# Performance work log

Hardware: AMD Instinct MI355X
Metric: run time of the kernel (lower is better)

## Reference

```python
import jax, jax.numpy as jnp
import numpy as np

B, NX, NC, C, H = 4, 1024, 2048, 1024, 16
DH = C // H            # head_dim = 64
SCALE = DH ** -0.5


def setup_inputs() -> dict:
    key = jax.random.key(0)
    ks = jax.random.split(key, 6)
    # sorted unique token indices to update per batch (== positions where update_mask==1)
    rng = np.random.default_rng(0)
    idx = np.stack([np.sort(rng.permutation(NC)[:NX]) for _ in range(B)]).astype(np.int32)
    return {
        "x": jax.random.normal(ks[0], (B, NX, C), jnp.float32),
        "update_idx": jnp.asarray(idx),                              # (B, NX) int32
        "cache_k": jax.random.normal(ks[1], (B, H, NC, DH), jnp.float32),
        "cache_v": jax.random.normal(ks[2], (B, H, NC, DH), jnp.float32),
        "w_qkv": jax.random.normal(ks[3], (3 * C, C), jnp.float32) * 0.02,
        "b_qkv": jnp.zeros((3 * C,), jnp.float32),
        "w_proj": jax.random.normal(ks[4], (C, C), jnp.float32) * 0.02,
        "b_proj": jnp.zeros((C,), jnp.float32),
    }


def reference(x, update_idx, cache_k, cache_v, w_qkv, b_qkv, w_proj, b_proj):
    Bq, N, Cq = x.shape
    # QKV projection: (B, N, 3C) -> (3, B, H, N, Dh) layout as in torch permute(2,0,3,1,4)
    qkv = (x @ w_qkv.T + b_qkv).reshape(Bq, N, 3, H, DH)
    q = qkv[:, :, 0].transpose(0, 2, 1, 3)  # (B, H, N, Dh)
    k = qkv[:, :, 1].transpose(0, 2, 1, 3)
    v = qkv[:, :, 2].transpose(0, 2, 1, 3)
    # masked_scatter_ of k/v into cache at the masked (updated) token slots.
    # Indices are sorted, so row-order masked_scatter == indexed scatter.
    scat = jax.vmap(lambda cache, idx, src: cache.at[:, idx, :].set(src))
    k_full = scat(cache_k, update_idx, k)    # (B, H, NC, Dh)
    v_full = scat(cache_v, update_idx, v)
    # plain attention: q scaled, full softmax over cache length
    attn = jax.nn.softmax(jnp.einsum('bhqd,bhkd->bhqk', q * SCALE, k_full), axis=-1)
    out = jnp.einsum('bhqk,bhkd->bhqd', attn, v_full)  # (B, H, N, Dh)
    out = out.transpose(0, 2, 1, 3).reshape(Bq, N, Cq)
    return out @ w_proj.T + b_proj
```

## Files before the change

kernel.cpp:

```cpp
#include <hip/hip_runtime.h>
#include <hip/hip_bf16.h>

#define B_   4
#define NX_  1024
#define NC_  2048
#define C_   1024
#define H_   16
#define DH_  64

typedef __attribute__((ext_vector_type(8))) __bf16 bf16x8;
typedef __attribute__((ext_vector_type(4))) float  f32x4;

static __device__ __forceinline__ unsigned short f2bf(float f) {
    unsigned int u = __float_as_uint(f);
    u += 0x7fffu + ((u >> 16) & 1u);
    return (unsigned short)(u >> 16);
}

static __device__ __forceinline__ unsigned int pk2(float lo, float hi) {
    unsigned int a = __float_as_uint(lo) + 0x8000u;
    unsigned int b = __float_as_uint(hi) + 0x8000u;
    return __builtin_amdgcn_perm(b, a, 0x07060302);
}

static __device__ __forceinline__ bf16x8 ldfrag(const unsigned short* p) {
    union { uint4 u; bf16x8 b; } cv;
    cv.u = *reinterpret_cast<const uint4*>(p);
    return cv.b;
}

__global__ __launch_bounds__(256) void cvt_all_kernel(
    const float* __restrict__ x,  const float* __restrict__ wq,
    const float* __restrict__ wp, const float* __restrict__ ck,
    const float* __restrict__ cv_,
    unsigned short* __restrict__ xbf,  unsigned short* __restrict__ wqbf,
    unsigned short* __restrict__ wpbf, unsigned short* __restrict__ kfb,
    unsigned short* __restrict__ vt) {
    int blk = blockIdx.x;
    if (blk < 16384) {
        const float* src; unsigned short* dst; int i;
        if (blk < 4096)      { src = x;  dst = xbf;  i = blk; }
        else if (blk < 7168) { src = wq; dst = wqbf; i = blk - 4096; }
        else if (blk < 8192) { src = wp; dst = wpbf; i = blk - 7168; }
        else                 { src = ck; dst = kfb;  i = blk - 8192; }
        int idx = i * 256 + threadIdx.x;
        float4 f = reinterpret_cast<const float4*>(src)[idx];
        ushort4 o;
        o.x = f2bf(f.x); o.y = f2bf(f.y); o.z = f2bf(f.z); o.w = f2bf(f.w);
        reinterpret_cast<ushort4*>(dst)[idx] = o;
    } else {
        int i   = blk - 16384;
        int t   = threadIdx.x;
        int bh  = i >> 6;
        int kg  = i & 63;
        int d   = t & 63;
        int kci = t >> 6;
        int kc  = kg * 4 + kci;
        const float* src = cv_ + ((size_t)bh * NC_ + (size_t)kc * 8) * DH_ + d;
        union { uint4 u; unsigned short s[8]; } o;
#pragma unroll
        for (int j = 0; j < 8; j++) o.s[j] = f2bf(src[(size_t)j * DH_]);
        *reinterpret_cast<uint4*>(vt + ((size_t)bh * DH_ + d) * NC_ + (size_t)kc * 8) = o.u;
    }
}

#define LSTR 40

__global__ __launch_bounds__(256, 3) void qkv_gemm_kernel(
    const unsigned short* __restrict__ xbf,
    const unsigned short* __restrict__ wbf,
    const float* __restrict__ bias,
    const int* __restrict__ uidx,
    unsigned short* __restrict__ qb,
    unsigned short* __restrict__ kf,
    unsigned short* __restrict__ vt)
{
    __shared__ unsigned short As[128 * LSTR], Bs[128 * LSTR];
    __shared__ int jtab[128];
    int bn = blockIdx.x, bm = blockIdx.y;
    int w = threadIdx.x >> 6, l = threadIdx.x & 63;
    int quad = l >> 4, col = l & 15;
    int wr = w >> 1, wc = w & 1;
    int srow = w * 32 + (l >> 2), schk = (l & 3) * 8;

    const unsigned short* Ap = xbf + (size_t)(bm * 128 + srow) * C_ + schk;
    const unsigned short* Bp = wbf + (size_t)(bn * 128 + srow) * C_ + schk;
    unsigned short* Aw = As + srow * LSTR + schk;
    unsigned short* Bw = Bs + srow * LSTR + schk;

    f32x4 acc[4][4];
#pragma unroll
    for (int a = 0; a < 4; a++)
#pragma unroll
        for (int b = 0; b < 4; b++) acc[a][b] = (f32x4){0.f, 0.f, 0.f, 0.f};

    uint4 ar0, ar1, br0, br1;
#define LDREG(kk_)                                                       \
    {   int kk = (kk_) * 32;                                             \
        ar0 = *reinterpret_cast<const uint4*>(Ap + kk);                  \
        ar1 = *reinterpret_cast<const uint4*>(Ap + 16 * C_ + kk);        \
        br0 = *reinterpret_cast<const uint4*>(Bp + kk);                  \
        br1 = *reinterpret_cast<const uint4*>(Bp + 16 * C_ + kk);        \
    }
#define WRTILE()                                                         \
    {   *reinterpret_cast<uint4*>(Aw)             = ar0;                 \
        *reinterpret_cast<uint4*>(Aw + 16 * LSTR) = ar1;                 \
        *reinterpret_cast<uint4*>(Bw)             = br0;                 \
        *reinterpret_cast<uint4*>(Bw + 16 * LSTR) = br1;                 \
    }

    LDREG(0);
    WRTILE();
    LDREG(1);
    __syncthreads();
#pragma unroll 1
    for (int it = 0; it < 32; it++) {
        bf16x8 af[4], bfr[4];
#pragma unroll
        for (int t = 0; t < 4; t++) af[t]  = ldfrag(&As[(wr * 64 + t * 16 + col) * LSTR + quad * 8]);
#pragma unroll
        for (int t = 0; t < 4; t++) bfr[t] = ldfrag(&Bs[(wc * 64 + t * 16 + col) * LSTR + quad * 8]);
#pragma unroll
        for (int mt = 0; mt < 4; mt++)
#pragma unroll
            for (int nt = 0; nt < 4; nt++)
                acc[mt][nt] = __builtin_amdgcn_mfma_f32_16x16x32_bf16(af[mt], bfr[nt], acc[mt][nt], 0, 0, 0);
        if (it < 31) {
            __syncthreads();
            WRTILE();
            LDREG(it + 2 < 31 ? it + 2 : 31);
            __syncthreads();
        }
    }
#undef LDREG
#undef WRTILE

    int part = bn >> 3;
    float bv[4];
#pragma unroll
    for (int nt = 0; nt < 4; nt++) bv[nt] = bias[bn * 128 + wc * 64 + nt * 16 + col];

    if (part <= 1) {
        int nl[4];
#pragma unroll
        for (int nt = 0; nt < 4; nt++) nl[nt] = (bn * 128 + wc * 64 + nt * 16 + col) & 1023;
        const float QS = 0.18033688011112042f;
#pragma unroll
        for (int mt = 0; mt < 4; mt++)
#pragma unroll
            for (int r = 0; r < 4; r++) {
                int m = bm * 128 + wr * 64 + mt * 16 + quad * 4 + r;
                int b = m >> 10, i = m & 1023;
                int j = (part == 0) ? 0 : uidx[m];
#pragma unroll
                for (int nt = 0; nt < 4; nt++) {
                    int h = nl[nt] >> 6, d = nl[nt] & 63;
                    float v = acc[mt][nt][r] + bv[nt];
                    if (part == 0)
                        qb[((size_t)(b * H_ + h) * NX_ + i) * DH_ + d] = f2bf(v * QS);
                    else
                        kf[((size_t)(b * H_ + h) * NC_ + j) * DH_ + d] = f2bf(v);
                }
            }
    } else {
        if (threadIdx.x < 128) jtab[threadIdx.x] = uidx[bm * 128 + threadIdx.x];
        __syncthreads();
        int h = ((bn * 128 + wc * 64) & 1023) >> 6;
        int b = (bm * 128) >> 10;
        unsigned short* T = (wc == 0) ? As : Bs;
        int jv = jtab[wr * 64 + l];
        unsigned short* vb2 = vt + ((size_t)(b * H_ + h) * 64) * NC_ + jv;
#pragma unroll 1
        for (int round = 0; round < 2; round++) {
            if (wr == round) {
#pragma unroll
                for (int nt = 0; nt < 4; nt++)
#pragma unroll
                    for (int mt = 0; mt < 4; mt++) {
                        uint2 pk;
                        pk.x = pk2(acc[mt][nt][0] + bv[nt], acc[mt][nt][1] + bv[nt]);
                        pk.y = pk2(acc[mt][nt][2] + bv[nt], acc[mt][nt][3] + bv[nt]);
                        *reinterpret_cast<uint2*>(&T[(nt * 16 + col) * 72 + mt * 16 + quad * 4]) = pk;
                    }
                asm volatile("s_waitcnt lgkmcnt(0)" ::: "memory");
#pragma unroll 1
                for (int d = 0; d < 64; d++)
                    vb2[(size_t)d * NC_] = T[d * 72 + l];
            }
            __syncthreads();
        }
    }
}

#define PST 40
__global__ __launch_bounds__(256, 4) void attn_kernel(
    const unsigned short* __restrict__ qb,
    const unsigned short* __restrict__ kf,
    const unsigned short* __restrict__ vt,
    unsigned short* __restrict__ ao)
{
    __shared__ __align__(16) char smem[20480 + 10240];
    unsigned short* Klo = (unsigned short*)smem;
    unsigned short* Khi = Klo + 64 * LSTR;
    unsigned short* V0s = Khi + 64 * LSTR;
    unsigned short* V1s = V0s + 64 * LSTR;
    unsigned short* Psh = (unsigned short*)(smem + 20480);
    float* Om = (float*)smem;
    float* Lm = Om + 2 * 32 * 64;

    int id = blockIdx.x;
    int qt = (id >> 3) & 15;
    int bh = ((id >> 7) << 3) | (id & 7);
    int wave = threadIdx.x >> 6, lane = threadIdx.x & 63;
    int quad = lane >> 4, col = lane & 15;
    int qh = wave & 1;
    int kh = wave >> 1;
    int srow = wave * 16 + (lane >> 2), schk = (lane & 3) * 8;

    const unsigned short* qrow0 = qb + ((size_t)bh * NX_ + qt * 64 + qh * 32 + col) * DH_;
    bf16x8 qfA[2], qfB[2];
    qfA[0] = ldfrag(qrow0 + quad * 8);
    qfB[0] = ldfrag(qrow0 + 32 + quad * 8);
    qfA[1] = ldfrag(qrow0 + 16 * DH_ + quad * 8);
    qfB[1] = ldfrag(qrow0 + 16 * DH_ + 32 + quad * 8);

    const unsigned short* Kp = kf + ((size_t)bh * NC_ + srow) * DH_ + schk;
    const unsigned short* Vp = vt + ((size_t)bh * DH_ + srow) * NC_ + schk;
    unsigned short* Kwl = Klo + srow * LSTR + schk;
    unsigned short* Kwh = Khi + srow * LSTR + schk;
    unsigned short* Vw0 = V0s + srow * LSTR + schk;
    unsigned short* Vw1 = V1s + srow * LSTR + schk;
    unsigned short* Pw0 = Psh + (wave * 2 + 0) * 16 * PST;
    unsigned short* Pw1 = Psh + (wave * 2 + 1) * 16 * PST;
    const unsigned short* Vs = kh ? V1s : V0s;
    int kq = kh * 32;

    f32x4 o[4][2];
#pragma unroll
    for (int m = 0; m < 4; m++)
#pragma unroll
        for (int n = 0; n < 2; n++) o[m][n] = (f32x4){0.f, 0.f, 0.f, 0.f};
    float l_i[2] = {0.f, 0.f};

    uint4 kr0, kr1, vr0, vr1;
#define LDREG(kb_)                                                        \
    {   kr0 = *reinterpret_cast<const uint4*>(Kp + (size_t)(kb_) * 64 * DH_);      \
        kr1 = *reinterpret_cast<const uint4*>(Kp + (size_t)(kb_) * 64 * DH_ + 32); \
        vr0 = *reinterpret_cast<const uint4*>(Vp + (kb_) * 64);           \
        vr1 = *reinterpret_cast<const uint4*>(Vp + (kb_) * 64 + 32);      \
    }
#define WRTILE()                                                          \
    {   *reinterpret_cast<uint4*>(Kwl) = kr0;                             \
        *reinterpret_cast<uint4*>(Kwh) = kr1;                             \
        *reinterpret_cast<uint4*>(Vw0) = vr0;                             \
        *reinterpret_cast<uint4*>(Vw1) = vr1;                             \
    }

    LDREG(0);
    WRTILE();
    LDREG(1);
    __syncthreads();

#pragma unroll 1
    for (int kb = 0; kb < 32; kb++) {
        f32x4 s[2][2];
#pragma unroll
        for (int mt = 0; mt < 2; mt++)
#pragma unroll
            for (int nt = 0; nt < 2; nt++) s[mt][nt] = (f32x4){0.f, 0.f, 0.f, 0.f};
#pragma unroll
        for (int mt = 0; mt < 2; mt++) {
            bf16x8 ka = ldfrag(&Klo[(kq + mt * 16 + col) * LSTR + quad * 8]);
            bf16x8 kb_ = ldfrag(&Khi[(kq + mt * 16 + col) * LSTR + quad * 8]);
#pragma unroll
            for (int nt = 0; nt < 2; nt++) {
                s[mt][nt] = __builtin_amdgcn_mfma_f32_16x16x32_bf16(ka,  qfA[nt], s[mt][nt], 0, 0, 0);
                s[mt][nt] = __builtin_amdgcn_mfma_f32_16x16x32_bf16(kb_, qfB[nt], s[mt][nt], 0, 0, 0);
            }
        }
        bf16x8 vfr[4];
#pragma unroll
        for (int t = 0; t < 4; t++) vfr[t] = ldfrag(&Vs[(t * 16 + col) * LSTR + quad * 8]);
#pragma unroll
        for (int nt = 0; nt < 2; nt++) {
            unsigned short* Pw = nt ? Pw1 : Pw0;
            float p0 = exp2f(s[0][nt][0]), p1 = exp2f(s[0][nt][1]);
            float p2 = exp2f(s[0][nt][2]), p3 = exp2f(s[0][nt][3]);
            float p4 = exp2f(s[1][nt][0]), p5 = exp2f(s[1][nt][1]);
            float p6 = exp2f(s[1][nt][2]), p7 = exp2f(s[1][nt][3]);
            l_i[nt] += ((p0 + p1) + (p2 + p3)) + ((p4 + p5) + (p6 + p7));
            uint2 w0; w0.x = pk2(p0, p1); w0.y = pk2(p2, p3);
            uint2 w1; w1.x = pk2(p4, p5); w1.y = pk2(p6, p7);
            *reinterpret_cast<uint2*>(&Pw[col * PST +      quad * 4]) = w0;
            *reinterpret_cast<uint2*>(&Pw[col * PST + 16 + quad * 4]) = w1;
        }
        asm volatile("" ::: "memory");
        {
            bf16x8 pf0 = ldfrag(&Pw0[col * PST + quad * 8]);
            bf16x8 pf1 = ldfrag(&Pw1[col * PST + quad * 8]);
#pragma unroll
            for (int mt = 0; mt < 4; mt++) {
                o[mt][0] = __builtin_amdgcn_mfma_f32_16x16x32_bf16(vfr[mt], pf0, o[mt][0], 0, 0, 0);
                o[mt][1] = __builtin_amdgcn_mfma_f32_16x16x32_bf16(vfr[mt], pf1, o[mt][1], 0, 0, 0);
            }
        }
        asm volatile("" ::: "memory");
        if (kb < 31) {
            __syncthreads();
            WRTILE();
            LDREG(kb + 2 < 31 ? kb + 2 : 31);
            __syncthreads();
        }
    }
#undef LDREG
#undef WRTILE

#pragma unroll
    for (int nt = 0; nt < 2; nt++) {
        l_i[nt] += __shfl_xor(l_i[nt], 16, 64);
        l_i[nt] += __shfl_xor(l_i[nt], 32, 64);
    }

    __syncthreads();
    if (kh == 1) {
#pragma unroll
        for (int mt = 0; mt < 4; mt++)
#pragma unroll
            for (int nt = 0; nt < 2; nt++)
#pragma unroll
                for (int r = 0; r < 4; r++)
                    Om[(qh * 32 + (mt * 2 + nt) * 4 + r) * 64 + lane] = o[mt][nt][r];
        if (quad == 0) {
            Lm[(qh * 2 + 0) * 16 + col] = l_i[0];
            Lm[(qh * 2 + 1) * 16 + col] = l_i[1];
        }
    }
    __syncthreads();
    if (kh == 0) {
        float inv[2];
#pragma unroll
        for (int nt = 0; nt < 2; nt++)
            inv[nt] = 1.f / (l_i[nt] + Lm[(qh * 2 + nt) * 16 + col]);
        int b = bh >> 4, h = bh & 15;
#pragma unroll
        for (int mt = 0; mt < 4; mt++)
#pragma unroll
            for (int nt = 0; nt < 2; nt++) {
                int base = (qh * 32 + (mt * 2 + nt) * 4) * 64 + lane;
                float v0 = (o[mt][nt][0] + Om[base])       * inv[nt];
                float v1 = (o[mt][nt][1] + Om[base + 64])  * inv[nt];
                float v2 = (o[mt][nt][2] + Om[base + 128]) * inv[nt];
                float v3 = (o[mt][nt][3] + Om[base + 192]) * inv[nt];
                int q = qt * 64 + qh * 32 + nt * 16 + col;
                uint2 ov;
                ov.x = pk2(v0, v1);
                ov.y = pk2(v2, v3);
                *reinterpret_cast<uint2*>(ao + ((size_t)b * NX_ + q) * C_ +
                                          h * 64 + mt * 16 + quad * 4) = ov;
            }
    }
}

__global__ __launch_bounds__(256, 3) void proj_gemm_kernel(
    const unsigned short* __restrict__ abf,
    const unsigned short* __restrict__ wbf,
    const float* __restrict__ bias,
    float* __restrict__ out)
{
    __shared__ unsigned short As[128 * LSTR], Bs[64 * LSTR];
    int bn = blockIdx.x, bm = blockIdx.y;
    int w = threadIdx.x >> 6, l = threadIdx.x & 63;
    int quad = l >> 4, col = l & 15;
    int sarow = w * 32 + (l >> 2), sbrow = w * 16 + (l >> 2), schk = (l & 3) * 8;

    const unsigned short* Ap = abf + (size_t)(bm * 128 + sarow) * C_ + schk;
    const unsigned short* Bp = wbf + (size_t)(bn * 64 + sbrow) * C_ + schk;
    unsigned short* Aw = As + sarow * LSTR + schk;
    unsigned short* Bw = Bs + sbrow * LSTR + schk;

    f32x4 acc[2][4];
#pragma unroll
    for (int a = 0; a < 2; a++)
#pragma unroll
        for (int b = 0; b < 4; b++) acc[a][b] = (f32x4){0.f, 0.f, 0.f, 0.f};

    uint4 ar0, ar1, br0;
#define LDREG(kk_)                                                       \
    {   int kk = (kk_) * 32;                                             \
        ar0 = *reinterpret_cast<const uint4*>(Ap + kk);                  \
        ar1 = *reinterpret_cast<const uint4*>(Ap + 16 * C_ + kk);        \
        br0 = *reinterpret_cast<const uint4*>(Bp + kk);                  \
    }
#define WRTILE()                                                         \
    {   *reinterpret_cast<uint4*>(Aw)             = ar0;                 \
        *reinterpret_cast<uint4*>(Aw + 16 * LSTR) = ar1;                 \
        *reinterpret_cast<uint4*>(Bw)             = br0;                 \
    }

    LDREG(0);
    WRTILE();
    LDREG(1);
    __syncthreads();
#pragma unroll 1
    for (int it = 0; it < 32; it++) {
        bf16x8 af[2], bfr[4];
#pragma unroll
        for (int t = 0; t < 2; t++) af[t]  = ldfrag(&As[(w * 32 + t * 16 + col) * LSTR + quad * 8]);
#pragma unroll
        for (int t = 0; t < 4; t++) bfr[t] = ldfrag(&Bs[(t * 16 + col) * LSTR + quad * 8]);
#pragma unroll
        for (int mt = 0; mt < 2; mt++)
#pragma unroll
            for (int nt = 0; nt < 4; nt++)
                acc[mt][nt] = __builtin_amdgcn_mfma_f32_16x16x32_bf16(af[mt], bfr[nt], acc[mt][nt], 0, 0, 0);
        if (it < 31) {
            __syncthreads();
            WRTILE();
            LDREG(it + 2 < 31 ? it + 2 : 31);
            __syncthreads();
        }
    }
#undef LDREG
#undef WRTILE

    float bv[4];
#pragma unroll
    for (int nt = 0; nt < 4; nt++) bv[nt] = bias[bn * 64 + nt * 16 + col];
#pragma unroll
    for (int mt = 0; mt < 2; mt++)
#pragma unroll
        for (int r = 0; r < 4; r++) {
            int m = bm * 128 + w * 32 + mt * 16 + quad * 4 + r;
#pragma unroll
            for (int nt = 0; nt < 4; nt++) {
                int n = bn * 64 + nt * 16 + col;
                out[(size_t)m * C_ + n] = acc[mt][nt][r] + bv[nt];
            }
        }
}

extern "C" void kernel_launch(void* const* d_in, const int* in_sizes, int n_in,
                              void* d_out, int out_size, void* d_ws, size_t ws_size,
                              hipStream_t stream) {
    const float* x      = (const float*)d_in[0];
    const int*   uidx   = (const int*)  d_in[1];
    const float* cachek = (const float*)d_in[2];
    const float* cachev = (const float*)d_in[3];
    const float* wqkv   = (const float*)d_in[4];
    const float* bqkv   = (const float*)d_in[5];
    const float* wproj  = (const float*)d_in[6];
    const float* bproj  = (const float*)d_in[7];
    float* out = (float*)d_out;

    char* ws = (char*)d_ws;
    unsigned short* xbf  = (unsigned short*)(ws);
    unsigned short* wqbf = (unsigned short*)(ws + (8ull  << 20));
    unsigned short* wpbf = (unsigned short*)(ws + (14ull << 20));
    unsigned short* qb   = (unsigned short*)(ws + (16ull << 20));
    unsigned short* kfb  = (unsigned short*)(ws + (24ull << 20));
    unsigned short* vtb  = (unsigned short*)(ws + (40ull << 20));
    unsigned short* aob  = (unsigned short*)(ws + (56ull << 20));

    cvt_all_kernel<<<20480, 256, 0, stream>>>(x, wqkv, wproj, cachek, cachev,
                                              xbf, wqbf, wpbf, kfb, vtb);
    qkv_gemm_kernel <<<dim3(24, 32), 256, 0, stream>>>(xbf, wqbf, bqkv, uidx, qb, kfb, vtb);
    attn_kernel     <<<1024, 256, 0, stream>>>(qb, kfb, vtb, aob);
    proj_gemm_kernel<<<dim3(16, 32), 256, 0, stream>>>(aob, wpbf, bproj, out);
}
```

Measured before the change: 266.7 us.

## Split attention keys across waves and load K/V fragments directly into registers

```diff
diff --git a/kernel.cpp b/kernel.cpp
--- a/kernel.cpp
+++ b/kernel.cpp
@@ -26,6 +26,12 @@
 static __device__ __forceinline__ bf16x8 ldfrag(const unsigned short* p) {
     union { uint4 u; bf16x8 b; } cv;
     cv.u = *reinterpret_cast<const uint4*>(p);
+    return cv.b;
+}
+
+static __device__ __forceinline__ bf16x8 asbf(uint4 u) {
+    union { uint4 u; bf16x8 b; } cv;
+    cv.u = u;
     return cv.b;
 }
 
@@ -193,165 +199,161 @@
 }
 
 #define PST 40
-__global__ __launch_bounds__(256, 4) void attn_kernel(
+__global__ __launch_bounds__(256, 2) void attn_kernel(
     const unsigned short* __restrict__ qb,
     const unsigned short* __restrict__ kf,
     const unsigned short* __restrict__ vt,
     unsigned short* __restrict__ ao)
 {
-    __shared__ __align__(16) char smem[20480 + 10240];
-    unsigned short* Klo = (unsigned short*)smem;
-    unsigned short* Khi = Klo + 64 * LSTR;
-    unsigned short* V0s = Khi + 64 * LSTR;
-    unsigned short* V1s = V0s + 64 * LSTR;
-    unsigned short* Psh = (unsigned short*)(smem + 20480);
+    __shared__ __align__(16) char smem[20480];
+    unsigned short* Psh = (unsigned short*)smem;
     float* Om = (float*)smem;
-    float* Lm = Om + 2 * 32 * 64;
+    float* Lm = Om + 64 * 64;
 
     int id = blockIdx.x;
     int qt = (id >> 3) & 15;
     int bh = ((id >> 7) << 3) | (id & 7);
     int wave = threadIdx.x >> 6, lane = threadIdx.x & 63;
     int quad = lane >> 4, col = lane & 15;
-    int qh = wave & 1;
-    int kh = wave >> 1;
-    int srow = wave * 16 + (lane >> 2), schk = (lane & 3) * 8;
-
-    const unsigned short* qrow0 = qb + ((size_t)bh * NX_ + qt * 64 + qh * 32 + col) * DH_;
-    bf16x8 qfA[2], qfB[2];
-    qfA[0] = ldfrag(qrow0 + quad * 8);
-    qfB[0] = ldfrag(qrow0 + 32 + quad * 8);
-    qfA[1] = ldfrag(qrow0 + 16 * DH_ + quad * 8);
-    qfB[1] = ldfrag(qrow0 + 16 * DH_ + 32 + quad * 8);
-
-    const unsigned short* Kp = kf + ((size_t)bh * NC_ + srow) * DH_ + schk;
-    const unsigned short* Vp = vt + ((size_t)bh * DH_ + srow) * NC_ + schk;
-    unsigned short* Kwl = Klo + srow * LSTR + schk;
-    unsigned short* Kwh = Khi + srow * LSTR + schk;
-    unsigned short* Vw0 = V0s + srow * LSTR + schk;
-    unsigned short* Vw1 = V1s + srow * LSTR + schk;
-    unsigned short* Pw0 = Psh + (wave * 2 + 0) * 16 * PST;
-    unsigned short* Pw1 = Psh + (wave * 2 + 1) * 16 * PST;
-    const unsigned short* Vs = kh ? V1s : V0s;
-    int kq = kh * 32;
-
-    f32x4 o[4][2];
+
+    const unsigned short* qp = qb + ((size_t)bh * NX_ + qt * 64 + col) * DH_ + quad * 8;
+    bf16x8 qf[4][2];
+#pragma unroll
+    for (int nt = 0; nt < 4; nt++) {
+        qf[nt][0] = ldfrag(qp + nt * 16 * DH_);
+        qf[nt][1] = ldfrag(qp + nt * 16 * DH_ + 32);
+    }
+
+    const unsigned short* Kp = kf + ((size_t)bh * NC_ + wave * 512 + col) * DH_ + quad * 8;
+    const unsigned short* Vp = vt + ((size_t)bh * DH_ + col) * NC_ + wave * 512 + quad * 8;
+    unsigned short* Pw = Psh + wave * (4 * 16 * PST);
+
+    f32x4 o[4][4];
 #pragma unroll
     for (int m = 0; m < 4; m++)
 #pragma unroll
-        for (int n = 0; n < 2; n++) o[m][n] = (f32x4){0.f, 0.f, 0.f, 0.f};
-    float l_i[2] = {0.f, 0.f};
-
-    uint4 kr0, kr1, vr0, vr1;
-#define LDREG(kb_)                                                        \
-    {   kr0 = *reinterpret_cast<const uint4*>(Kp + (size_t)(kb_) * 64 * DH_);      \
-        kr1 = *reinterpret_cast<const uint4*>(Kp + (size_t)(kb_) * 64 * DH_ + 32); \
-        vr0 = *reinterpret_cast<const uint4*>(Vp + (kb_) * 64);           \
-        vr1 = *reinterpret_cast<const uint4*>(Vp + (kb_) * 64 + 32);      \
-    }
-#define WRTILE()                                                          \
-    {   *reinterpret_cast<uint4*>(Kwl) = kr0;                             \
-        *reinterpret_cast<uint4*>(Kwh) = kr1;                             \
-        *reinterpret_cast<uint4*>(Vw0) = vr0;                             \
-        *reinterpret_cast<uint4*>(Vw1) = vr1;                             \
-    }
-
-    LDREG(0);
-    WRTILE();
-    LDREG(1);
-    __syncthreads();
-
-#pragma unroll 1
-    for (int kb = 0; kb < 32; kb++) {
-        f32x4 s[2][2];
-#pragma unroll
-        for (int mt = 0; mt < 2; mt++)
-#pragma unroll
-            for (int nt = 0; nt < 2; nt++) s[mt][nt] = (f32x4){0.f, 0.f, 0.f, 0.f};
-#pragma unroll
-        for (int mt = 0; mt < 2; mt++) {
-            bf16x8 ka = ldfrag(&Klo[(kq + mt * 16 + col) * LSTR + quad * 8]);
-            bf16x8 kb_ = ldfrag(&Khi[(kq + mt * 16 + col) * LSTR + quad * 8]);
-#pragma unroll
-            for (int nt = 0; nt < 2; nt++) {
-                s[mt][nt] = __builtin_amdgcn_mfma_f32_16x16x32_bf16(ka,  qfA[nt], s[mt][nt], 0, 0, 0);
-                s[mt][nt] = __builtin_amdgcn_mfma_f32_16x16x32_bf16(kb_, qfB[nt], s[mt][nt], 0, 0, 0);
-            }
-        }
-        bf16x8 vfr[4];
-#pragma unroll
-        for (int t = 0; t < 4; t++) vfr[t] = ldfrag(&Vs[(t * 16 + col) * LSTR + quad * 8]);
-#pragma unroll
-        for (int nt = 0; nt < 2; nt++) {
-            unsigned short* Pw = nt ? Pw1 : Pw0;
-            float p0 = exp2f(s[0][nt][0]), p1 = exp2f(s[0][nt][1]);
-            float p2 = exp2f(s[0][nt][2]), p3 = exp2f(s[0][nt][3]);
-            float p4 = exp2f(s[1][nt][0]), p5 = exp2f(s[1][nt][1]);
-            float p6 = exp2f(s[1][nt][2]), p7 = exp2f(s[1][nt][3]);
+        for (int n = 0; n < 4; n++) o[m][n] = (f32x4){0.f, 0.f, 0.f, 0.f};
+    float l_i[4] = {0.f, 0.f, 0.f, 0.f};
+
+    uint4 ka[4], kn[4], vr[4];
+#define LOADK(D, kb_) {                                                                  \
+    const unsigned short* kp_ = Kp + (size_t)(kb_) * 32 * DH_;                           \
+    D[0] = *reinterpret_cast<const uint4*>(kp_);                                         \
+    D[1] = *reinterpret_cast<const uint4*>(kp_ + 32);                                    \
+    D[2] = *reinterpret_cast<const uint4*>(kp_ + 16 * DH_);                              \
+    D[3] = *reinterpret_cast<const uint4*>(kp_ + 16 * DH_ + 32); }
+#define LOADV(kb_) {                                                                     \
+    const unsigned short* vp_ = Vp + (size_t)(kb_) * 32;                                 \
+    vr[0] = *reinterpret_cast<const uint4*>(vp_);                                        \
+    vr[1] = *reinterpret_cast<const uint4*>(vp_ + 16 * NC_);                             \
+    vr[2] = *reinterpret_cast<const uint4*>(vp_ + 32 * NC_);                             \
+    vr[3] = *reinterpret_cast<const uint4*>(vp_ + 48 * NC_); }
+
+    auto step = [&](const uint4 (&kc)[4]) {
+#pragma unroll
+        for (int nt = 0; nt < 4; nt++) {
+            f32x4 s0 = (f32x4){0.f, 0.f, 0.f, 0.f};
+            f32x4 s1 = (f32x4){0.f, 0.f, 0.f, 0.f};
+            s0 = __builtin_amdgcn_mfma_f32_16x16x32_bf16(asbf(kc[0]), qf[nt][0], s0, 0, 0, 0);
+            s0 = __builtin_amdgcn_mfma_f32_16x16x32_bf16(asbf(kc[1]), qf[nt][1], s0, 0, 0, 0);
+            s1 = __builtin_amdgcn_mfma_f32_16x16x32_bf16(asbf(kc[2]), qf[nt][0], s1, 0, 0, 0);
+            s1 = __builtin_amdgcn_mfma_f32_16x16x32_bf16(asbf(kc[3]), qf[nt][1], s1, 0, 0, 0);
+            float p0 = exp2f(s0[0]), p1 = exp2f(s0[1]), p2 = exp2f(s0[2]), p3 = exp2f(s0[3]);
+            float p4 = exp2f(s1[0]), p5 = exp2f(s1[1]), p6 = exp2f(s1[2]), p7 = exp2f(s1[3]);
             l_i[nt] += ((p0 + p1) + (p2 + p3)) + ((p4 + p5) + (p6 + p7));
             uint2 w0; w0.x = pk2(p0, p1); w0.y = pk2(p2, p3);
             uint2 w1; w1.x = pk2(p4, p5); w1.y = pk2(p6, p7);
-            *reinterpret_cast<uint2*>(&Pw[col * PST +      quad * 4]) = w0;
-            *reinterpret_cast<uint2*>(&Pw[col * PST + 16 + quad * 4]) = w1;
+            *reinterpret_cast<uint2*>(&Pw[nt * 16 * PST + col * PST +      quad * 4]) = w0;
+            *reinterpret_cast<uint2*>(&Pw[nt * 16 * PST + col * PST + 16 + quad * 4]) = w1;
         }
         asm volatile("" ::: "memory");
-        {
-            bf16x8 pf0 = ldfrag(&Pw0[col * PST + quad * 8]);
-            bf16x8 pf1 = ldfrag(&Pw1[col * PST + quad * 8]);
-#pragma unroll
-            for (int mt = 0; mt < 4; mt++) {
-                o[mt][0] = __builtin_amdgcn_mfma_f32_16x16x32_bf16(vfr[mt], pf0, o[mt][0], 0, 0, 0);
-                o[mt][1] = __builtin_amdgcn_mfma_f32_16x16x32_bf16(vfr[mt], pf1, o[mt][1], 0, 0, 0);
-            }
+#pragma unroll
+        for (int nt = 0; nt < 4; nt++) {
+            bf16x8 pf = ldfrag(&Pw[nt * 16 * PST + col * PST + quad * 8]);
+            o[0][nt] = __builtin_amdgcn_mfma_f32_16x16x32_bf16(asbf(vr[0]), pf, o[0][nt], 0, 0, 0);
+            o[1][nt] = __builtin_amdgcn_mfma_f32_16x16x32_bf16(asbf(vr[1]), pf, o[1][nt], 0, 0, 0);
+            o[2][nt] = __builtin_amdgcn_mfma_f32_16x16x32_bf16(asbf(vr[2]), pf, o[2][nt], 0, 0, 0);
+            o[3][nt] = __builtin_amdgcn_mfma_f32_16x16x32_bf16(asbf(vr[3]), pf, o[3][nt], 0, 0, 0);
         }
         asm volatile("" ::: "memory");
-        if (kb < 31) {
-            __syncthreads();
-            WRTILE();
-            LDREG(kb + 2 < 31 ? kb + 2 : 31);
-            __syncthreads();
-        }
-    }
-#undef LDREG
-#undef WRTILE
-
-#pragma unroll
-    for (int nt = 0; nt < 2; nt++) {
+    };
+
+    LOADK(ka, 0);
+#pragma unroll 1
+    for (int kb = 0; kb < 16; kb += 2) {
+        LOADV(kb);
+        LOADK(kn, kb + 1);
+        step(ka);
+        LOADV(kb + 1);
+        int nx = (kb + 2 < 16) ? kb + 2 : 15;
+        LOADK(ka, nx);
+        step(kn);
+    }
+#undef LOADK
+#undef LOADV
+
+#pragma unroll
+    for (int nt = 0; nt < 4; nt++) {
         l_i[nt] += __shfl_xor(l_i[nt], 16, 64);
         l_i[nt] += __shfl_xor(l_i[nt], 32, 64);
     }
 
     __syncthreads();
-    if (kh == 1) {
-#pragma unroll
-        for (int mt = 0; mt < 4; mt++)
-#pragma unroll
-            for (int nt = 0; nt < 2; nt++)
+    if (wave == 3) {
+#pragma unroll
+        for (int mt = 0; mt < 4; mt++)
+#pragma unroll
+            for (int nt = 0; nt < 4; nt++)
 #pragma unroll
                 for (int r = 0; r < 4; r++)
-                    Om[(qh * 32 + (mt * 2 + nt) * 4 + r) * 64 + lane] = o[mt][nt][r];
-        if (quad == 0) {
-            Lm[(qh * 2 + 0) * 16 + col] = l_i[0];
-            Lm[(qh * 2 + 1) * 16 + col] = l_i[1];
-        }
-    }
-    __syncthreads();
-    if (kh == 0) {
-        float inv[2];
-#pragma unroll
-        for (int nt = 0; nt < 2; nt++)
-            inv[nt] = 1.f / (l_i[nt] + Lm[(qh * 2 + nt) * 16 + col]);
+                    Om[((mt * 4 + nt) * 4 + r) * 64 + lane] = o[mt][nt][r];
+        if (quad == 0)
+#pragma unroll
+            for (int nt = 0; nt < 4; nt++) Lm[nt * 16 + col] = l_i[nt];
+    }
+    __syncthreads();
+    if (wave == 2) {
+#pragma unroll
+        for (int mt = 0; mt < 4; mt++)
+#pragma unroll
+            for (int nt = 0; nt < 4; nt++)
+#pragma unroll
+                for (int r = 0; r < 4; r++)
+                    Om[((mt * 4 + nt) * 4 + r) * 64 + lane] += o[mt][nt][r];
+        if (quad == 0)
+#pragma unroll
+            for (int nt = 0; nt < 4; nt++) Lm[nt * 16 + col] += l_i[nt];
+    }
+    __syncthreads();
+    if (wave == 1) {
+#pragma unroll
+        for (int mt = 0; mt < 4; mt++)
+#pragma unroll
+            for (int nt = 0; nt < 4; nt++)
+#pragma unroll
+                for (int r = 0; r < 4; r++)
+                    Om[((mt * 4 + nt) * 4 + r) * 64 + lane] += o[mt][nt][r];
+        if (quad == 0)
+#pragma unroll
+            for (int nt = 0; nt < 4; nt++) Lm[nt * 16 + col] += l_i[nt];
+    }
+    __syncthreads();
+    if (wave == 0) {
+        float inv[4];
+#pragma unroll
+        for (int nt = 0; nt < 4; nt++)
+            inv[nt] = 1.f / (l_i[nt] + Lm[nt * 16 + col]);
         int b = bh >> 4, h = bh & 15;
 #pragma unroll
         for (int mt = 0; mt < 4; mt++)
 #pragma unroll
-            for (int nt = 0; nt < 2; nt++) {
-                int base = (qh * 32 + (mt * 2 + nt) * 4) * 64 + lane;
-                float v0 = (o[mt][nt][0] + Om[base])       * inv[nt];
-                float v1 = (o[mt][nt][1] + Om[base + 64])  * inv[nt];
+            for (int nt = 0; nt < 4; nt++) {
+                int base = ((mt * 4 + nt) * 4) * 64 + lane;
+                float v0 = (o[mt][nt][0] + Om[base      ]) * inv[nt];
+                float v1 = (o[mt][nt][1] + Om[base +  64]) * inv[nt];
                 float v2 = (o[mt][nt][2] + Om[base + 128]) * inv[nt];
                 float v3 = (o[mt][nt][3] + Om[base + 192]) * inv[nt];
-                int q = qt * 64 + qh * 32 + nt * 16 + col;
+                int q = qt * 64 + nt * 16 + col;
                 uint2 ov;
                 ov.x = pk2(v0, v1);
                 ov.y = pk2(v2, v3);
```

After: 272.3 us. +2.1%, slower.

## Feed softmax probabilities to PV MFMA from registers via permuted V layout

Applied to the files above, without the earlier changes.

```diff
diff --git a/kernel.cpp b/kernel.cpp
--- a/kernel.cpp
+++ b/kernel.cpp
@@ -192,19 +192,17 @@
     }
 }
 
-#define PST 40
 __global__ __launch_bounds__(256, 4) void attn_kernel(
     const unsigned short* __restrict__ qb,
     const unsigned short* __restrict__ kf,
     const unsigned short* __restrict__ vt,
     unsigned short* __restrict__ ao)
 {
-    __shared__ __align__(16) char smem[20480 + 10240];
+    __shared__ __align__(16) char smem[20480];
     unsigned short* Klo = (unsigned short*)smem;
     unsigned short* Khi = Klo + 64 * LSTR;
     unsigned short* V0s = Khi + 64 * LSTR;
     unsigned short* V1s = V0s + 64 * LSTR;
-    unsigned short* Psh = (unsigned short*)(smem + 20480);
     float* Om = (float*)smem;
     float* Lm = Om + 2 * 32 * 64;
 
@@ -216,6 +214,9 @@
     int qh = wave & 1;
     int kh = wave >> 1;
     int srow = wave * 16 + (lane >> 2), schk = (lane & 3) * 8;
+    int L = lane & 3;
+    int ve0 = (L < 2) ? 16 * L : 16 * L - 28;
+    int ve1 = ve0 + 8;
 
     const unsigned short* qrow0 = qb + ((size_t)bh * NX_ + qt * 64 + qh * 32 + col) * DH_;
     bf16x8 qfA[2], qfB[2];
@@ -228,10 +229,8 @@
     const unsigned short* Vp = vt + ((size_t)bh * DH_ + srow) * NC_ + schk;
     unsigned short* Kwl = Klo + srow * LSTR + schk;
     unsigned short* Kwh = Khi + srow * LSTR + schk;
-    unsigned short* Vw0 = V0s + srow * LSTR + schk;
-    unsigned short* Vw1 = V1s + srow * LSTR + schk;
-    unsigned short* Pw0 = Psh + (wave * 2 + 0) * 16 * PST;
-    unsigned short* Pw1 = Psh + (wave * 2 + 1) * 16 * PST;
+    unsigned short* Vw0 = V0s + srow * LSTR;
+    unsigned short* Vw1 = V1s + srow * LSTR;
     const unsigned short* Vs = kh ? V1s : V0s;
     int kq = kh * 32;
 
@@ -252,8 +251,11 @@
 #define WRTILE()                                                          \
     {   *reinterpret_cast<uint4*>(Kwl) = kr0;                             \
         *reinterpret_cast<uint4*>(Kwh) = kr1;                             \
-        *reinterpret_cast<uint4*>(Vw0) = vr0;                             \
-        *reinterpret_cast<uint4*>(Vw1) = vr1;                             \
+        uint2 t_;                                                         \
+        t_.x = vr0.x; t_.y = vr0.y; *reinterpret_cast<uint2*>(Vw0 + ve0) = t_; \
+        t_.x = vr0.z; t_.y = vr0.w; *reinterpret_cast<uint2*>(Vw0 + ve1) = t_; \
+        t_.x = vr1.x; t_.y = vr1.y; *reinterpret_cast<uint2*>(Vw1 + ve0) = t_; \
+        t_.x = vr1.z; t_.y = vr1.w; *reinterpret_cast<uint2*>(Vw1 + ve1) = t_; \
     }
 
     LDREG(0);
@@ -281,30 +283,26 @@
         bf16x8 vfr[4];
 #pragma unroll
         for (int t = 0; t < 4; t++) vfr[t] = ldfrag(&Vs[(t * 16 + col) * LSTR + quad * 8]);
+        bf16x8 pf[2];
 #pragma unroll
         for (int nt = 0; nt < 2; nt++) {
-            unsigned short* Pw = nt ? Pw1 : Pw0;
             float p0 = exp2f(s[0][nt][0]), p1 = exp2f(s[0][nt][1]);
             float p2 = exp2f(s[0][nt][2]), p3 = exp2f(s[0][nt][3]);
             float p4 = exp2f(s[1][nt][0]), p5 = exp2f(s[1][nt][1]);
             float p6 = exp2f(s[1][nt][2]), p7 = exp2f(s[1][nt][3]);
             l_i[nt] += ((p0 + p1) + (p2 + p3)) + ((p4 + p5) + (p6 + p7));
-            uint2 w0; w0.x = pk2(p0, p1); w0.y = pk2(p2, p3);
-            uint2 w1; w1.x = pk2(p4, p5); w1.y = pk2(p6, p7);
-            *reinterpret_cast<uint2*>(&Pw[col * PST +      quad * 4]) = w0;
-            *reinterpret_cast<uint2*>(&Pw[col * PST + 16 + quad * 4]) = w1;
-        }
-        asm volatile("" ::: "memory");
-        {
-            bf16x8 pf0 = ldfrag(&Pw0[col * PST + quad * 8]);
-            bf16x8 pf1 = ldfrag(&Pw1[col * PST + quad * 8]);
-#pragma unroll
-            for (int mt = 0; mt < 4; mt++) {
-                o[mt][0] = __builtin_amdgcn_mfma_f32_16x16x32_bf16(vfr[mt], pf0, o[mt][0], 0, 0, 0);
-                o[mt][1] = __builtin_amdgcn_mfma_f32_16x16x32_bf16(vfr[mt], pf1, o[mt][1], 0, 0, 0);
-            }
-        }
-        asm volatile("" ::: "memory");
+            union { unsigned int u[4]; bf16x8 b; } pw;
+            pw.u[0] = pk2(p0, p1);
+            pw.u[1] = pk2(p2, p3);
+            pw.u[2] = pk2(p4, p5);
+            pw.u[3] = pk2(p6, p7);
+            pf[nt] = pw.b;
+        }
+#pragma unroll
+        for (int mt = 0; mt < 4; mt++) {
+            o[mt][0] = __builtin_amdgcn_mfma_f32_16x16x32_bf16(vfr[mt], pf[0], o[mt][0], 0, 0, 0);
+            o[mt][1] = __builtin_amdgcn_mfma_f32_16x16x32_bf16(vfr[mt], pf[1], o[mt][1], 0, 0, 0);
+        }
         if (kb < 31) {
             __syncthreads();
             WRTILE();
```

Result: faster. 256.5 us (-3.9%).
